# Performance work log

Hardware: AMD Instinct MI355X
Metric: run time of the kernel (lower is better)

The kernel has to match this reference:

```python
import jax, jax.numpy as jnp
import numpy as np

B, C, H, W = 32, 512, 64, 64
K = 32  # num_codes


def setup_inputs() -> dict:
    key = jax.random.key(0)
    k1, k2, k3 = jax.random.split(key, 3)
    x = jax.random.normal(k1, (B, C, H, W), dtype=jnp.float32)
    std = 1.0 / (K * C) ** 0.5
    codewords = jax.random.uniform(k2, (K, C), dtype=jnp.float32, minval=-std, maxval=std)
    scale = jax.random.uniform(k3, (K,), dtype=jnp.float32, minval=-1.0, maxval=0.0)
    return {"x": x, "codewords": codewords, "scale": scale}


def reference(x, codewords, scale):
    # x: [B, C, H, W] -> [B, N, C] with N = H*W
    b, c = x.shape[0], x.shape[1]
    xf = x.reshape(b, c, -1).transpose(0, 2, 1)  # [B, N, C]
    # scaled L2: scale_k * ||x_n - c_k||^2, expanded algebraically to avoid [B,N,K,C]
    x2 = jnp.sum(xf * xf, axis=-1)                      # [B, N]
    c2 = jnp.sum(codewords * codewords, axis=-1)        # [K]
    xc = jnp.einsum('bnc,kc->bnk', xf, codewords)       # [B, N, K]
    dist = scale[None, None, :] * (x2[:, :, None] - 2.0 * xc + c2[None, None, :])
    w = jax.nn.softmax(dist, axis=2)                    # [B, N, K]
    # aggregate: sum_n w_{nk} * (x_n - c_k) = (w^T x) - (sum_n w_{nk}) * c_k
    wx = jnp.einsum('bnk,bnc->bkc', w, xf)              # [B, K, C]
    wsum = jnp.sum(w, axis=1)                           # [B, K]
    encoded_feat = wx - wsum[:, :, None] * codewords[None, :, :]  # [B, K, C]
    return encoded_feat
```

## Files before the change

### kernel.cpp

```cpp
#include <hip/hip_runtime.h>
#include <stdint.h>

#define Bdim 32
#define Cdim 512
#define Ndim 4096
#define Kdim 32
#define NPX 32
#define NCH 16
#define PWIN 8

static constexpr size_t WS_WSUM_OFF = (size_t)256 * Kdim * Cdim * 4;
static constexpr size_t WS_C2_OFF   = WS_WSUM_OFF + (size_t)256 * Kdim * 4;

using bf16x8 = __attribute__((ext_vector_type(8))) short;
using f32x4  = __attribute__((ext_vector_type(4))) float;

static __device__ __forceinline__ unsigned short f2bf(float f) {
    unsigned int u = __float_as_uint(f);
    u += 0x7fffu + ((u >> 16) & 1u);
    return (unsigned short)(u >> 16);
}

__global__ __launch_bounds__(256) void k0_c2(const float* __restrict__ cw,
                                             float* __restrict__ c2) {
    __shared__ float partl[8][32];
    int t = threadIdx.x;
    int k = t & 31, g = t >> 5;
    float s = 0.f;
    int c0 = g * 64;
    for (int c = c0; c < c0 + 64; ++c) {
        float v = cw[k * Cdim + c];
        s += v * v;
    }
    partl[g][k] = s;
    __syncthreads();
    if (t < 32) {
        float tot = 0.f;
        #pragma unroll
        for (int gg = 0; gg < 8; ++gg) tot += partl[gg][t];
        c2[t] = tot;
    }
}

__global__ __launch_bounds__(256) void k1_fused(const float* __restrict__ x,
                                                const float* __restrict__ cw,
                                                const float* __restrict__ scale,
                                                const float* __restrict__ c2g,
                                                float* __restrict__ part,
                                                float* __restrict__ wsum_part) {
    __shared__ unsigned short cw_s[Kdim][520];
    __shared__ unsigned short x_n[NPX][520];
    __shared__ unsigned short x_t[Cdim][40];
    __shared__ float          S_s[NPX][36];
    __shared__ unsigned short w_t[Kdim][40];
    __shared__ float          x2_s[NPX];
    __shared__ float          wsum_s[Kdim];

    const int t    = threadIdx.x;
    const int blk  = blockIdx.x;
    const int b    = blk >> 3;
    const int pw   = blk & 7;
    const int lane = t & 63;
    const int lr   = lane & 15;
    const int lq   = lane >> 4;
    const int wv   = t >> 6;
    const int q    = t & 7;
    const int px   = t >> 3;

    if (t < 32) { x2_s[t] = 0.f; wsum_s[t] = 0.f; }

    #pragma unroll
    for (int i = 0; i < 16; ++i) {
        int f4 = t + 256 * i;
        int k  = f4 >> 7;
        int c4 = (f4 & 127) * 4;
        float4 v = *(const float4*)(cw + (size_t)k * Cdim + c4);
        ushort4 u;
        u.x = f2bf(v.x); u.y = f2bf(v.y); u.z = f2bf(v.z); u.w = f2bf(v.w);
        *(ushort4*)&cw_s[k][c4] = u;
    }

    const float4 sc4 = *(const float4*)(scale + 4 * q);
    const float4 c24 = *(const float4*)(c2g + 4 * q);

    const float* xb = x + (size_t)b * Cdim * Ndim;

    float4 pa[8], pb[8];
    {
        int n0 = pw * 512;
        #pragma unroll
        for (int i = 0; i < 8; ++i) {
            int c = 2 * px + 64 * i;
            pa[i] = *(const float4*)(xb + (size_t)c * Ndim + n0 + 4 * q);
            pb[i] = *(const float4*)(xb + (size_t)(c + 1) * Ndim + n0 + 4 * q);
        }
    }

    f32x4 acc[2][8];
    #pragma unroll
    for (int kt = 0; kt < 2; ++kt)
        #pragma unroll
        for (int ct = 0; ct < 8; ++ct) acc[kt][ct] = (f32x4){0.f, 0.f, 0.f, 0.f};
    float wsum_r[4] = {0.f, 0.f, 0.f, 0.f};

    __syncthreads();

    for (int ci = 0; ci < NCH; ++ci) {
        float x2p[4] = {0.f, 0.f, 0.f, 0.f};
        #pragma unroll
        for (int i = 0; i < 8; ++i) {
            int c = 2 * px + 64 * i;
            float4 a = pa[i], bb = pb[i];
            ushort4 ua, ub;
            ua.x = f2bf(a.x);  ua.y = f2bf(a.y);  ua.z = f2bf(a.z);  ua.w = f2bf(a.w);
            ub.x = f2bf(bb.x); ub.y = f2bf(bb.y); ub.z = f2bf(bb.z); ub.w = f2bf(bb.w);
            *(ushort4*)&x_t[c][4 * q]     = ua;
            *(ushort4*)&x_t[c + 1][4 * q] = ub;
            ushort2 p0; p0.x = ua.x; p0.y = ub.x; *(ushort2*)&x_n[4 * q + 0][c] = p0;
            ushort2 p1; p1.x = ua.y; p1.y = ub.y; *(ushort2*)&x_n[4 * q + 1][c] = p1;
            ushort2 p2; p2.x = ua.z; p2.y = ub.z; *(ushort2*)&x_n[4 * q + 2][c] = p2;
            ushort2 p3; p3.x = ua.w; p3.y = ub.w; *(ushort2*)&x_n[4 * q + 3][c] = p3;
            x2p[0] += a.x * a.x + bb.x * bb.x;
            x2p[1] += a.y * a.y + bb.y * bb.y;
            x2p[2] += a.z * a.z + bb.z * bb.z;
            x2p[3] += a.w * a.w + bb.w * bb.w;
        }
        #pragma unroll
        for (int j = 0; j < 4; ++j) {
            float v = x2p[j];
            v += __shfl_xor(v, 8);
            v += __shfl_xor(v, 16);
            v += __shfl_xor(v, 32);
            if (lane < 8) atomicAdd(&x2_s[4 * q + j], v);
        }
        if (ci + 1 < NCH) {
            int nn = pw * 512 + (ci + 1) * 32;
            #pragma unroll
            for (int i = 0; i < 8; ++i) {
                int c = 2 * px + 64 * i;
                pa[i] = *(const float4*)(xb + (size_t)c * Ndim + nn + 4 * q);
                pb[i] = *(const float4*)(xb + (size_t)(c + 1) * Ndim + nn + 4 * q);
            }
        }
        __syncthreads();

        {
            const int pt = wv & 1, kt2 = wv >> 1;
            f32x4 d = (f32x4){0.f, 0.f, 0.f, 0.f};
            #pragma unroll
            for (int s = 0; s < 16; ++s) {
                bf16x8 av = *(const bf16x8*)&x_n[16 * pt + lr][32 * s + 8 * lq];
                bf16x8 bv = *(const bf16x8*)&cw_s[16 * kt2 + lr][32 * s + 8 * lq];
                d = __builtin_amdgcn_mfma_f32_16x16x32_bf16(av, bv, d, 0, 0, 0);
            }
            #pragma unroll
            for (int r = 0; r < 4; ++r)
                S_s[16 * pt + 4 * lq + r][16 * kt2 + lr] = d[r];
        }
        __syncthreads();

        {
            float4 dv = *(const float4*)&S_s[px][4 * q];
            float xx = x2_s[px];
            float d0 = sc4.x * (xx - 2.f * dv.x + c24.x);
            float d1 = sc4.y * (xx - 2.f * dv.y + c24.y);
            float d2 = sc4.z * (xx - 2.f * dv.z + c24.z);
            float d3 = sc4.w * (xx - 2.f * dv.w + c24.w);
            float m = fmaxf(fmaxf(d0, d1), fmaxf(d2, d3));
            m = fmaxf(m, __shfl_xor(m, 1));
            m = fmaxf(m, __shfl_xor(m, 2));
            m = fmaxf(m, __shfl_xor(m, 4));
            float e0 = __expf(d0 - m), e1 = __expf(d1 - m);
            float e2 = __expf(d2 - m), e3 = __expf(d3 - m);
            float ss = e0 + e1 + e2 + e3;
            ss += __shfl_xor(ss, 1);
            ss += __shfl_xor(ss, 2);
            ss += __shfl_xor(ss, 4);
            float inv = 1.f / ss;
            float w0 = e0 * inv, w1 = e1 * inv, w2 = e2 * inv, w3 = e3 * inv;
            wsum_r[0] += w0; wsum_r[1] += w1; wsum_r[2] += w2; wsum_r[3] += w3;
            w_t[4 * q + 0][px] = f2bf(w0);
            w_t[4 * q + 1][px] = f2bf(w1);
            w_t[4 * q + 2][px] = f2bf(w2);
            w_t[4 * q + 3][px] = f2bf(w3);
        }
        __syncthreads();

        {
            const int c0w = 128 * wv;
            bf16x8 a0 = *(const bf16x8*)&w_t[lr][8 * lq];
            bf16x8 a1 = *(const bf16x8*)&w_t[16 + lr][8 * lq];
            if (t < 32) x2_s[t] = 0.f;
            #pragma unroll
            for (int ct = 0; ct < 8; ++ct) {
                bf16x8 bv = *(const bf16x8*)&x_t[c0w + 16 * ct + lr][8 * lq];
                acc[0][ct] = __builtin_amdgcn_mfma_f32_16x16x32_bf16(a0, bv, acc[0][ct], 0, 0, 0);
                acc[1][ct] = __builtin_amdgcn_mfma_f32_16x16x32_bf16(a1, bv, acc[1][ct], 0, 0, 0);
            }
        }
        __syncthreads();
    }

    #pragma unroll
    for (int j = 0; j < 4; ++j) {
        float v = wsum_r[j];
        v += __shfl_xor(v, 8);
        v += __shfl_xor(v, 16);
        v += __shfl_xor(v, 32);
        if (lane < 8) atomicAdd(&wsum_s[4 * q + j], v);
    }
    {
        const int c0w = 128 * wv;
        float* pbuf = part + (size_t)blk * (Kdim * Cdim);
        #pragma unroll
        for (int kt = 0; kt < 2; ++kt)
            #pragma unroll
            for (int ct = 0; ct < 8; ++ct)
                #pragma unroll
                for (int r = 0; r < 4; ++r)
                    pbuf[(size_t)(16 * kt + 4 * lq + r) * Cdim + c0w + 16 * ct + lr] =
                        acc[kt][ct][r];
    }
    __syncthreads();
    if (t < 32) wsum_part[blk * Kdim + t] = wsum_s[t];
}

__global__ __launch_bounds__(256) void k2_reduce(const float* __restrict__ part,
                                                 const float* __restrict__ wsum_part,
                                                 const float* __restrict__ cw,
                                                 float* __restrict__ out) {
    int blk = blockIdx.x;
    int b = blk >> 5, k = blk & 31;
    int t = threadIdx.x;
    float ws = 0.f;
    #pragma unroll
    for (int p = 0; p < PWIN; ++p) ws += wsum_part[(b * PWIN + p) * Kdim + k];
    int c = 2 * t;
    float sx = 0.f, sy = 0.f;
    #pragma unroll
    for (int p = 0; p < PWIN; ++p) {
        const float2 v = *(const float2*)(part + ((size_t)(b * PWIN + p) * Kdim + k) * Cdim + c);
        sx += v.x;
        sy += v.y;
    }
    float2 cv = *(const float2*)(cw + (size_t)k * Cdim + c);
    float2 o;
    o.x = sx - ws * cv.x;
    o.y = sy - ws * cv.y;
    *(float2*)(out + ((size_t)b * Kdim + k) * Cdim + c) = o;
}

extern "C" void kernel_launch(void* const* d_in, const int* in_sizes, int n_in,
                              void* d_out, int out_size, void* d_ws, size_t ws_size,
                              hipStream_t stream) {
    const float* x     = (const float*)d_in[0];
    const float* cw    = (const float*)d_in[1];
    const float* scale = (const float*)d_in[2];
    float* out = (float*)d_out;

    char* wsb = (char*)d_ws;
    float* part      = (float*)wsb;
    float* wsum_part = (float*)(wsb + WS_WSUM_OFF);
    float* c2        = (float*)(wsb + WS_C2_OFF);

    k0_c2<<<1, 256, 0, stream>>>(cw, c2);
    k1_fused<<<Bdim * PWIN, 256, 0, stream>>>(x, cw, scale, c2, part, wsum_part);
    k2_reduce<<<Bdim * Kdim, 256, 0, stream>>>(part, wsum_part, cw, out);
}
```

Before: 384.4 us.

## Double fused kernel block size to 512 threads and split distance MFMA over channels

The fused kernel now runs 512 threads per block instead of 256. Each thread loads float2 instead of float4 of x, the distance GEMM is split across two channel halves whose partial results are summed through a doubled S_s buffer, and each wave in the aggregation GEMM covers 64 channels instead of 128. Shared-memory atomics for x2 and wsum are replaced by per-wave slots that are summed afterwards. The aim is more waves per CU to hide global-load latency over a grid of only 256 blocks. The cost is that half the threads sit idle during the softmax phase and shared memory use grows slightly.

Result: no change. 381.6 us (-0.7%).

```diff
diff --git a/kernel.cpp b/kernel.cpp
--- a/kernel.cpp
+++ b/kernel.cpp
@@ -42,19 +42,19 @@
     }
 }
 
-__global__ __launch_bounds__(256) void k1_fused(const float* __restrict__ x,
-                                                const float* __restrict__ cw,
-                                                const float* __restrict__ scale,
-                                                const float* __restrict__ c2g,
-                                                float* __restrict__ part,
-                                                float* __restrict__ wsum_part) {
+__global__ __launch_bounds__(512, 2) void k1_fused(const float* __restrict__ x,
+                                                   const float* __restrict__ cw,
+                                                   const float* __restrict__ scale,
+                                                   const float* __restrict__ c2g,
+                                                   float* __restrict__ part,
+                                                   float* __restrict__ wsum_part) {
     __shared__ unsigned short cw_s[Kdim][520];
     __shared__ unsigned short x_n[NPX][520];
     __shared__ unsigned short x_t[Cdim][40];
-    __shared__ float          S_s[NPX][36];
+    __shared__ float          S_s[2][NPX][36];
     __shared__ unsigned short w_t[Kdim][40];
-    __shared__ float          x2_s[NPX];
-    __shared__ float          wsum_s[Kdim];
+    __shared__ float          x2_w[8][NPX];
+    __shared__ float          wsum_w[4][Kdim];
 
     const int t    = threadIdx.x;
     const int blk  = blockIdx.x;
@@ -64,14 +64,17 @@
     const int lr   = lane & 15;
     const int lq   = lane >> 4;
     const int wv   = t >> 6;
+    const int pp   = t & 15;
+    const int crg  = t >> 4;
     const int q    = t & 7;
     const int px   = t >> 3;
-
-    if (t < 32) { x2_s[t] = 0.f; wsum_s[t] = 0.f; }
-
-    #pragma unroll
-    for (int i = 0; i < 16; ++i) {
-        int f4 = t + 256 * i;
+    const int pt   = wv & 1;
+    const int kt2  = (wv >> 1) & 1;
+    const int ch   = wv >> 2;
+
+    #pragma unroll
+    for (int i = 0; i < 8; ++i) {
+        int f4 = t + 512 * i;
         int k  = f4 >> 7;
         int c4 = (f4 & 127) * 4;
         float4 v = *(const float4*)(cw + (size_t)k * Cdim + c4);
@@ -80,92 +83,92 @@
         *(ushort4*)&cw_s[k][c4] = u;
     }
 
-    const float4 sc4 = *(const float4*)(scale + 4 * q);
-    const float4 c24 = *(const float4*)(c2g + 4 * q);
+    float4 sc4, c24;
+    if (t < 256) {
+        sc4 = *(const float4*)(scale + 4 * q);
+        c24 = *(const float4*)(c2g + 4 * q);
+    }
 
     const float* xb = x + (size_t)b * Cdim * Ndim;
 
-    float4 pa[8], pb[8];
+    float2 pa[8], pb[8];
     {
         int n0 = pw * 512;
         #pragma unroll
         for (int i = 0; i < 8; ++i) {
-            int c = 2 * px + 64 * i;
-            pa[i] = *(const float4*)(xb + (size_t)c * Ndim + n0 + 4 * q);
-            pb[i] = *(const float4*)(xb + (size_t)(c + 1) * Ndim + n0 + 4 * q);
-        }
-    }
-
-    f32x4 acc[2][8];
+            int c = 2 * crg + 64 * i;
+            pa[i] = *(const float2*)(xb + (size_t)c * Ndim + n0 + 2 * pp);
+            pb[i] = *(const float2*)(xb + (size_t)(c + 1) * Ndim + n0 + 2 * pp);
+        }
+    }
+
+    f32x4 acc[2][4];
     #pragma unroll
     for (int kt = 0; kt < 2; ++kt)
         #pragma unroll
-        for (int ct = 0; ct < 8; ++ct) acc[kt][ct] = (f32x4){0.f, 0.f, 0.f, 0.f};
+        for (int ct = 0; ct < 4; ++ct) acc[kt][ct] = (f32x4){0.f, 0.f, 0.f, 0.f};
     float wsum_r[4] = {0.f, 0.f, 0.f, 0.f};
 
     __syncthreads();
 
     for (int ci = 0; ci < NCH; ++ci) {
-        float x2p[4] = {0.f, 0.f, 0.f, 0.f};
+        float x2p0 = 0.f, x2p1 = 0.f;
         #pragma unroll
         for (int i = 0; i < 8; ++i) {
-            int c = 2 * px + 64 * i;
-            float4 a = pa[i], bb = pb[i];
-            ushort4 ua, ub;
-            ua.x = f2bf(a.x);  ua.y = f2bf(a.y);  ua.z = f2bf(a.z);  ua.w = f2bf(a.w);
-            ub.x = f2bf(bb.x); ub.y = f2bf(bb.y); ub.z = f2bf(bb.z); ub.w = f2bf(bb.w);
-            *(ushort4*)&x_t[c][4 * q]     = ua;
-            *(ushort4*)&x_t[c + 1][4 * q] = ub;
-            ushort2 p0; p0.x = ua.x; p0.y = ub.x; *(ushort2*)&x_n[4 * q + 0][c] = p0;
-            ushort2 p1; p1.x = ua.y; p1.y = ub.y; *(ushort2*)&x_n[4 * q + 1][c] = p1;
-            ushort2 p2; p2.x = ua.z; p2.y = ub.z; *(ushort2*)&x_n[4 * q + 2][c] = p2;
-            ushort2 p3; p3.x = ua.w; p3.y = ub.w; *(ushort2*)&x_n[4 * q + 3][c] = p3;
-            x2p[0] += a.x * a.x + bb.x * bb.x;
-            x2p[1] += a.y * a.y + bb.y * bb.y;
-            x2p[2] += a.z * a.z + bb.z * bb.z;
-            x2p[3] += a.w * a.w + bb.w * bb.w;
-        }
-        #pragma unroll
-        for (int j = 0; j < 4; ++j) {
-            float v = x2p[j];
-            v += __shfl_xor(v, 8);
-            v += __shfl_xor(v, 16);
-            v += __shfl_xor(v, 32);
-            if (lane < 8) atomicAdd(&x2_s[4 * q + j], v);
+            int c = 2 * crg + 64 * i;
+            float2 a = pa[i], bb = pb[i];
+            unsigned short ax = f2bf(a.x), ay = f2bf(a.y);
+            unsigned short bx = f2bf(bb.x), by = f2bf(bb.y);
+            ushort2 u;
+            u.x = ax; u.y = ay; *(ushort2*)&x_t[c][2 * pp] = u;
+            u.x = bx; u.y = by; *(ushort2*)&x_t[c + 1][2 * pp] = u;
+            u.x = ax; u.y = bx; *(ushort2*)&x_n[2 * pp][c] = u;
+            u.x = ay; u.y = by; *(ushort2*)&x_n[2 * pp + 1][c] = u;
+            x2p0 += a.x * a.x + bb.x * bb.x;
+            x2p1 += a.y * a.y + bb.y * bb.y;
+        }
+        x2p0 += __shfl_xor(x2p0, 16); x2p1 += __shfl_xor(x2p1, 16);
+        x2p0 += __shfl_xor(x2p0, 32); x2p1 += __shfl_xor(x2p1, 32);
+        if (lane < 16) {
+            float2 v; v.x = x2p0; v.y = x2p1;
+            *(float2*)&x2_w[wv][2 * pp] = v;
         }
         if (ci + 1 < NCH) {
             int nn = pw * 512 + (ci + 1) * 32;
             #pragma unroll
             for (int i = 0; i < 8; ++i) {
-                int c = 2 * px + 64 * i;
-                pa[i] = *(const float4*)(xb + (size_t)c * Ndim + nn + 4 * q);
-                pb[i] = *(const float4*)(xb + (size_t)(c + 1) * Ndim + nn + 4 * q);
+                int c = 2 * crg + 64 * i;
+                pa[i] = *(const float2*)(xb + (size_t)c * Ndim + nn + 2 * pp);
+                pb[i] = *(const float2*)(xb + (size_t)(c + 1) * Ndim + nn + 2 * pp);
             }
         }
         __syncthreads();
 
         {
-            const int pt = wv & 1, kt2 = wv >> 1;
             f32x4 d = (f32x4){0.f, 0.f, 0.f, 0.f};
             #pragma unroll
-            for (int s = 0; s < 16; ++s) {
-                bf16x8 av = *(const bf16x8*)&x_n[16 * pt + lr][32 * s + 8 * lq];
-                bf16x8 bv = *(const bf16x8*)&cw_s[16 * kt2 + lr][32 * s + 8 * lq];
+            for (int s = 0; s < 8; ++s) {
+                int col = 256 * ch + 32 * s + 8 * lq;
+                bf16x8 av = *(const bf16x8*)&x_n[16 * pt + lr][col];
+                bf16x8 bv = *(const bf16x8*)&cw_s[16 * kt2 + lr][col];
                 d = __builtin_amdgcn_mfma_f32_16x16x32_bf16(av, bv, d, 0, 0, 0);
             }
             #pragma unroll
             for (int r = 0; r < 4; ++r)
-                S_s[16 * pt + 4 * lq + r][16 * kt2 + lr] = d[r];
-        }
-        __syncthreads();
-
-        {
-            float4 dv = *(const float4*)&S_s[px][4 * q];
-            float xx = x2_s[px];
-            float d0 = sc4.x * (xx - 2.f * dv.x + c24.x);
-            float d1 = sc4.y * (xx - 2.f * dv.y + c24.y);
-            float d2 = sc4.z * (xx - 2.f * dv.z + c24.z);
-            float d3 = sc4.w * (xx - 2.f * dv.w + c24.w);
+                S_s[ch][16 * pt + 4 * lq + r][16 * kt2 + lr] = d[r];
+        }
+        __syncthreads();
+
+        if (t < 256) {
+            float4 dv0 = *(const float4*)&S_s[0][px][4 * q];
+            float4 dv1 = *(const float4*)&S_s[1][px][4 * q];
+            float xx = 0.f;
+            #pragma unroll
+            for (int w = 0; w < 8; ++w) xx += x2_w[w][px];
+            float d0 = sc4.x * (xx - 2.f * (dv0.x + dv1.x) + c24.x);
+            float d1 = sc4.y * (xx - 2.f * (dv0.y + dv1.y) + c24.y);
+            float d2 = sc4.z * (xx - 2.f * (dv0.z + dv1.z) + c24.z);
+            float d3 = sc4.w * (xx - 2.f * (dv0.w + dv1.w) + c24.w);
             float m = fmaxf(fmaxf(d0, d1), fmaxf(d2, d3));
             m = fmaxf(m, __shfl_xor(m, 1));
             m = fmaxf(m, __shfl_xor(m, 2));
@@ -187,13 +190,11 @@
         __syncthreads();
 
         {
-            const int c0w = 128 * wv;
             bf16x8 a0 = *(const bf16x8*)&w_t[lr][8 * lq];
             bf16x8 a1 = *(const bf16x8*)&w_t[16 + lr][8 * lq];
-            if (t < 32) x2_s[t] = 0.f;
-            #pragma unroll
-            for (int ct = 0; ct < 8; ++ct) {
-                bf16x8 bv = *(const bf16x8*)&x_t[c0w + 16 * ct + lr][8 * lq];
+            #pragma unroll
+            for (int ct = 0; ct < 4; ++ct) {
+                bf16x8 bv = *(const bf16x8*)&x_t[64 * wv + 16 * ct + lr][8 * lq];
                 acc[0][ct] = __builtin_amdgcn_mfma_f32_16x16x32_bf16(a0, bv, acc[0][ct], 0, 0, 0);
                 acc[1][ct] = __builtin_amdgcn_mfma_f32_16x16x32_bf16(a1, bv, acc[1][ct], 0, 0, 0);
             }
@@ -201,28 +202,32 @@
         __syncthreads();
     }
 
-    #pragma unroll
-    for (int j = 0; j < 4; ++j) {
-        float v = wsum_r[j];
-        v += __shfl_xor(v, 8);
-        v += __shfl_xor(v, 16);
-        v += __shfl_xor(v, 32);
-        if (lane < 8) atomicAdd(&wsum_s[4 * q + j], v);
+    if (t < 256) {
+        #pragma unroll
+        for (int j = 0; j < 4; ++j) {
+            float v = wsum_r[j];
+            v += __shfl_xor(v, 8);
+            v += __shfl_xor(v, 16);
+            v += __shfl_xor(v, 32);
+            if (lane < 8) wsum_w[wv][4 * lane + j] = v;
+        }
     }
     {
-        const int c0w = 128 * wv;
         float* pbuf = part + (size_t)blk * (Kdim * Cdim);
         #pragma unroll
         for (int kt = 0; kt < 2; ++kt)
             #pragma unroll
-            for (int ct = 0; ct < 8; ++ct)
+            for (int ct = 0; ct < 4; ++ct)
                 #pragma unroll
                 for (int r = 0; r < 4; ++r)
-                    pbuf[(size_t)(16 * kt + 4 * lq + r) * Cdim + c0w + 16 * ct + lr] =
+                    pbuf[(size_t)(16 * kt + 4 * lq + r) * Cdim + 64 * wv + 16 * ct + lr] =
                         acc[kt][ct][r];
     }
     __syncthreads();
-    if (t < 32) wsum_part[blk * Kdim + t] = wsum_s[t];
+    if (t < 32) {
+        float s = wsum_w[0][t] + wsum_w[1][t] + wsum_w[2][t] + wsum_w[3][t];
+        wsum_part[blk * Kdim + t] = s;
+    }
 }
 
 __global__ __launch_bounds__(256) void k2_reduce(const float* __restrict__ part,
@@ -264,6 +269,6 @@
     float* c2        = (float*)(wsb + WS_C2_OFF);
 
     k0_c2<<<1, 256, 0, stream>>>(cw, c2);
-    k1_fused<<<Bdim * PWIN, 256, 0, stream>>>(x, cw, scale, c2, part, wsum_part);
+    k1_fused<<<Bdim * PWIN, 512, 0, stream>>>(x, cw, scale, c2, part, wsum_part);
     k2_reduce<<<Bdim * Kdim, 256, 0, stream>>>(part, wsum_part, cw, out);
 }
```
